# Performance work log

Hardware: AMD Instinct MI355X
Metric: run time of the kernel (lower is better)

## Reference

```python
import jax, jax.numpy as jnp
import numpy as np

N = 50000
E = 800000
D = 128
L = 2


def setup_inputs() -> dict:
    key = jax.random.key(0)
    ks = jax.random.split(key, 8)
    x = jax.random.normal(ks[0], (N, D), dtype=jnp.float32)
    edge_index = jax.random.randint(ks[1], (2, E), 0, N, dtype=jnp.int64)
    s = 1.0 / np.sqrt(D)
    Wl = jax.random.uniform(ks[2], (L, D, D), jnp.float32, -s, s)  # neighbor transform (with bias)
    bl = jax.random.uniform(ks[3], (L, D), jnp.float32, -s, s)
    Wr = jax.random.uniform(ks[4], (L, D, D), jnp.float32, -s, s)  # root/self transform (no bias)
    W = jax.random.uniform(ks[5], (D, D), jnp.float32, -s, s)      # final Linear
    b = jax.random.uniform(ks[6], (D,), jnp.float32, -s, s)
    return {"x": x, "edge_index": edge_index, "Wl": Wl, "bl": bl, "Wr": Wr, "W": W, "b": b}


def reference(x, edge_index, Wl, bl, Wr, W, b):
    src, dst = edge_index[0], edge_index[1]
    n = x.shape[0]
    for l in range(Wl.shape[0]):
        # gather neighbor (source) features, scatter-max into destination nodes
        agg = jax.ops.segment_max(x[src], dst, num_segments=n)  # [N, D]
        agg = jnp.where(jnp.isneginf(agg), 0.0, agg)  # PyG: isolated nodes -> 0
        # SAGEConv: lin_l(agg) + lin_r(x)
        x = agg @ Wl[l].T + bl[l] + x @ Wr[l].T
        x = jax.nn.relu(x)
    return x @ W.T + b
```

## Files before the change

kernel.cpp:

```cpp
#include <hip/hip_runtime.h>
#include <math.h>

#define NN 50000
#define NE 800000
#define DD 128
#define NBUCK 196
#define PTILE 4096
#define PBLOCKS 196
#define CONVB 6250

typedef unsigned short u16;
typedef short s8v __attribute__((ext_vector_type(8)));
typedef float f16v __attribute__((ext_vector_type(16)));

__device__ __forceinline__ u16 f2bf(float f) {
    unsigned u = __float_as_uint(f);
    return (u16)((u + 0x7FFFu + ((u >> 16) & 1u)) >> 16);
}
__device__ __forceinline__ float bflo(unsigned u) { return __uint_as_float(u << 16); }
__device__ __forceinline__ float bfhi(unsigned u) { return __uint_as_float(u & 0xFFFF0000u); }

__device__ __forceinline__ void pack_one(const float* __restrict__ Wl,
                                         const float* __restrict__ Wr,
                                         bool two, int o, u16* __restrict__ out) {
    int j = o & 7;
    int l = (o >> 3) & 63;
    int cn = o >> 9;
    int n = cn & 3;
    int c = cn >> 2;
    int colj = n * 32 + (l & 31);
    int k = c * 16 + (l >> 5) * 8 + j;
    float v;
    if (two) v = (k < DD) ? Wl[colj * DD + k] : Wr[colj * DD + (k - DD)];
    else     v = Wl[colj * DD + k];
    out[o] = f2bf(v);
}

__global__ __launch_bounds__(256) void prep_kernel(
        const float4* __restrict__ x4, ushort4* __restrict__ hb0,
        const float* __restrict__ Wl, const float* __restrict__ Wr,
        const float* __restrict__ W,
        u16* __restrict__ Bpk0, u16* __restrict__ Bpk1, u16* __restrict__ Bpkf,
        int* __restrict__ bcnt) {
    int bid = blockIdx.x;
    int tid = threadIdx.x;
    if (bid < CONVB) {
        int i = bid * 256 + tid;
        float4 v = x4[i];
        ushort4 o;
        o.x = f2bf(v.x); o.y = f2bf(v.y); o.z = f2bf(v.z); o.w = f2bf(v.w);
        hb0[i] = o;
    } else if (bid < CONVB + 128) {
        pack_one(Wl, Wr, true, (bid - CONVB) * 256 + tid, Bpk0);
    } else if (bid < CONVB + 256) {
        pack_one(Wl + DD * DD, Wr + DD * DD, true, (bid - CONVB - 128) * 256 + tid, Bpk1);
    } else if (bid < CONVB + 320) {
        pack_one(W, W, false, (bid - CONVB - 256) * 256 + tid, Bpkf);
    } else {
        if (tid < NBUCK) bcnt[tid] = 0;
    }
}

__global__ __launch_bounds__(256) void bucket_hist(const int* __restrict__ ei,
                                                   int* __restrict__ bcnt) {
    __shared__ int h[NBUCK];
    for (int i = threadIdx.x; i < NBUCK; i += 256) h[i] = 0;
    __syncthreads();
    int e0 = blockIdx.x * PTILE;
#pragma unroll
    for (int i = 0; i < 16; i++) {
        int e = e0 + i * 256 + threadIdx.x;
        if (e < NE) atomicAdd(&h[ei[NE + e] >> 8], 1);
    }
    __syncthreads();
    for (int i = threadIdx.x; i < NBUCK; i += 256)
        if (h[i]) atomicAdd(&bcnt[i], h[i]);
}

__global__ __launch_bounds__(256) void bucket_scan(const int* __restrict__ bcnt,
                                                   int* __restrict__ bbase,
                                                   int* __restrict__ bcur,
                                                   int* __restrict__ rowptr) {
    __shared__ int s[256];
    int t = threadIdx.x;
    int v = (t < NBUCK) ? bcnt[t] : 0;
    s[t] = v;
    __syncthreads();
    for (int o = 1; o < 256; o <<= 1) {
        int u = (t >= o) ? s[t - o] : 0;
        __syncthreads();
        s[t] += u;
        __syncthreads();
    }
    int ex = s[t] - v;
    if (t < NBUCK) { bbase[t] = ex; bcur[t] = ex; }
    if (t == 0) rowptr[NN] = NE;
}

__global__ __launch_bounds__(256) void bucket_partition(const int* __restrict__ ei,
                                                        int* __restrict__ bcur,
                                                        unsigned* __restrict__ packed) {
    __shared__ int h[NBUCK];
    __shared__ int base[NBUCK];
    int t = threadIdx.x;
    for (int i = t; i < NBUCK; i += 256) h[i] = 0;
    __syncthreads();
    int e0 = blockIdx.x * PTILE;
    int dsts[16], srcs[16];
#pragma unroll
    for (int i = 0; i < 16; i++) {
        int e = e0 + i * 256 + t;
        if (e < NE) {
            dsts[i] = ei[NE + e];
            srcs[i] = ei[e];
            atomicAdd(&h[dsts[i] >> 8], 1);
        } else dsts[i] = -1;
    }
    __syncthreads();
    for (int i = t; i < NBUCK; i += 256) {
        int c = h[i];
        base[i] = c ? atomicAdd(&bcur[i], c) : 0;
    }
    __syncthreads();
    for (int i = t; i < NBUCK; i += 256) h[i] = 0;
    __syncthreads();
#pragma unroll
    for (int i = 0; i < 16; i++) {
        if (dsts[i] >= 0) {
            int bk = dsts[i] >> 8;
            int r = atomicAdd(&h[bk], 1);
            packed[base[bk] + r] = (unsigned)srcs[i] | ((unsigned)(dsts[i] & 255) << 16);
        }
    }
}

__global__ __launch_bounds__(256) void bucket_csr(const unsigned* __restrict__ packed,
                                                  const int* __restrict__ bcnt,
                                                  const int* __restrict__ bbase,
                                                  int* __restrict__ rowptr,
                                                  int* __restrict__ col) {
    __shared__ int deg[256];
    __shared__ int off[256];
    int bk = blockIdx.x;
    int cnt = bcnt[bk], base = bbase[bk];
    int t = threadIdx.x;
    deg[t] = 0;
    __syncthreads();
    for (int i = t; i < cnt; i += 256) atomicAdd(&deg[packed[base + i] >> 16], 1);
    __syncthreads();
    int v = deg[t];
    off[t] = v;
    __syncthreads();
    for (int o = 1; o < 256; o <<= 1) {
        int u = (t >= o) ? off[t - o] : 0;
        __syncthreads();
        off[t] += u;
        __syncthreads();
    }
    int ex = off[t] - v;
    int node = (bk << 8) + t;
    if (node < NN) rowptr[node] = base + ex;
    deg[t] = ex;
    __syncthreads();
    for (int i = t; i < cnt; i += 256) {
        unsigned p = packed[base + i];
        int dl = p >> 16;
        int r = atomicAdd(&deg[dl], 1);
        col[base + r] = (int)(p & 0xFFFFu);
    }
}

__device__ __forceinline__ void vmax8(float* m, uint4 v) {
    m[0] = fmaxf(m[0], bflo(v.x)); m[1] = fmaxf(m[1], bfhi(v.x));
    m[2] = fmaxf(m[2], bflo(v.y)); m[3] = fmaxf(m[3], bfhi(v.y));
    m[4] = fmaxf(m[4], bflo(v.z)); m[5] = fmaxf(m[5], bfhi(v.z));
    m[6] = fmaxf(m[6], bflo(v.w)); m[7] = fmaxf(m[7], bfhi(v.w));
}

__global__ __launch_bounds__(256) void agg_kernel_bf(const uint4* __restrict__ xb4,
                                                     const int* __restrict__ row_ptr,
                                                     const int* __restrict__ col,
                                                     uint4* __restrict__ aggb4) {
    int node = blockIdx.x * 16 + (threadIdx.x >> 4);
    if (node >= NN) return;
    int j = threadIdx.x & 15;
    int s0 = row_ptr[node], s1 = row_ptr[node + 1];
    if (s0 == s1) {
        aggb4[(size_t)node * 16 + j] = make_uint4(0, 0, 0, 0);
        return;
    }
    float m0[8], m1[8], m2[8], m3[8];
#pragma unroll
    for (int q = 0; q < 8; q++) { m0[q] = m1[q] = m2[q] = m3[q] = -INFINITY; }
    int i = s0;
    for (; i + 8 <= s1; i += 8) {
        int c0 = col[i],     c1 = col[i + 1], c2 = col[i + 2], c3 = col[i + 3];
        int c4 = col[i + 4], c5 = col[i + 5], c6 = col[i + 6], c7 = col[i + 7];
        uint4 v0 = xb4[(size_t)c0 * 16 + j];
        uint4 v1 = xb4[(size_t)c1 * 16 + j];
        uint4 v2 = xb4[(size_t)c2 * 16 + j];
        uint4 v3 = xb4[(size_t)c3 * 16 + j];
        uint4 v4 = xb4[(size_t)c4 * 16 + j];
        uint4 v5 = xb4[(size_t)c5 * 16 + j];
        uint4 v6 = xb4[(size_t)c6 * 16 + j];
        uint4 v7 = xb4[(size_t)c7 * 16 + j];
        vmax8(m0, v0); vmax8(m1, v1); vmax8(m2, v2); vmax8(m3, v3);
        vmax8(m0, v4); vmax8(m1, v5); vmax8(m2, v6); vmax8(m3, v7);
    }
    for (; i + 4 <= s1; i += 4) {
        int c0 = col[i], c1 = col[i + 1], c2 = col[i + 2], c3 = col[i + 3];
        uint4 v0 = xb4[(size_t)c0 * 16 + j];
        uint4 v1 = xb4[(size_t)c1 * 16 + j];
        uint4 v2 = xb4[(size_t)c2 * 16 + j];
        uint4 v3 = xb4[(size_t)c3 * 16 + j];
        vmax8(m0, v0); vmax8(m1, v1); vmax8(m2, v2); vmax8(m3, v3);
    }
    for (; i < s1; i++) {
        uint4 v = xb4[(size_t)col[i] * 16 + j];
        vmax8(m0, v);
    }
#pragma unroll
    for (int q = 0; q < 8; q++) m0[q] = fmaxf(fmaxf(m0[q], m1[q]), fmaxf(m2[q], m3[q]));
    uint4 o;
    o.x = (__float_as_uint(m0[0]) >> 16) | (__float_as_uint(m0[1]) & 0xFFFF0000u);
    o.y = (__float_as_uint(m0[2]) >> 16) | (__float_as_uint(m0[3]) & 0xFFFF0000u);
    o.z = (__float_as_uint(m0[4]) >> 16) | (__float_as_uint(m0[5]) & 0xFFFF0000u);
    o.w = (__float_as_uint(m0[6]) >> 16) | (__float_as_uint(m0[7]) & 0xFFFF0000u);
    aggb4[(size_t)node * 16 + j] = o;
}

template<int NKC16, bool TWO_SRC, bool RELU, bool OUT_BF16>
__global__ __launch_bounds__(256) void mfma_gemm(const u16* __restrict__ srcA,
                                                 const u16* __restrict__ srcB,
                                                 const u16* __restrict__ Bpk,
                                                 const float* __restrict__ bias,
                                                 void* __restrict__ outv) {
    int tid = threadIdx.x;
    int wt = tid >> 6;
    int lane = tid & 63;
    int row0 = blockIdx.x * 128 + wt * 32;
    int rload = row0 + (lane & 31);
    if (rload > NN - 1) rload = NN - 1;
    int koff = (lane >> 5) * 8;
    const s8v* Bv = (const s8v*)Bpk;

    f16v acc[4];
#pragma unroll
    for (int n = 0; n < 4; n++) acc[n] = (f16v)(0.0f);

#pragma unroll
    for (int c = 0; c < NKC16; c++) {
        const u16* s = srcA;
        int kk = c * 16;
        if (TWO_SRC && c >= 8) { s = srcB; kk = (c - 8) * 16; }
        s8v a = *(const s8v*)(s + (size_t)rload * DD + kk + koff);
#pragma unroll
        for (int n = 0; n < 4; n++) {
            s8v b = Bv[(c * 4 + n) * 64 + lane];
            acc[n] = __builtin_amdgcn_mfma_f32_32x32x16_bf16(a, b, acc[n], 0, 0, 0);
        }
    }

    int rowadd = 4 * (lane >> 5);
#pragma unroll
    for (int n = 0; n < 4; n++) {
        int colj = n * 32 + (lane & 31);
        float bj = bias[colj];
#pragma unroll
        for (int r = 0; r < 16; r++) {
            int row = row0 + (r & 3) + 8 * (r >> 2) + rowadd;
            if (row < NN) {
                float v = acc[n][r] + bj;
                if (RELU) v = fmaxf(v, 0.0f);
                if (OUT_BF16) ((u16*)outv)[(size_t)row * DD + colj] = f2bf(v);
                else          ((float*)outv)[(size_t)row * DD + colj] = v;
            }
        }
    }
}

extern "C" void kernel_launch(void* const* d_in, const int* in_sizes, int n_in,
                              void* d_out, int out_size, void* d_ws, size_t ws_size,
                              hipStream_t stream) {
    const float* x  = (const float*)d_in[0];
    const int*   ei = (const int*)d_in[1];
    const float* Wl = (const float*)d_in[2];
    const float* bl = (const float*)d_in[3];
    const float* Wr = (const float*)d_in[4];
    const float* W  = (const float*)d_in[5];
    const float* b  = (const float*)d_in[6];
    float* out = (float*)d_out;

    u16* aggb = (u16*)d_ws;
    u16* hb0  = aggb + (size_t)NN * DD;
    u16* hb1  = hb0 + (size_t)NN * DD;
    u16* Bpk0 = hb1 + (size_t)NN * DD;
    u16* Bpk1 = Bpk0 + 32768;
    u16* Bpkf = Bpk1 + 32768;
    unsigned* packed = (unsigned*)(Bpkf + 16384);
    int* col    = (int*)(packed + NE);
    int* rowptr = col + NE;
    int* bcnt   = rowptr + NN + 1;
    int* bbase  = bcnt + NBUCK;
    int* bcur   = bbase + NBUCK;

    dim3 blk(256);
    int gemmBlocks = (NN + 127) / 128;
    int aggBlocks  = (NN + 15) / 16;
    int prepBlocks = CONVB + 320 + 1;

    prep_kernel<<<prepBlocks, blk, 0, stream>>>(
        (const float4*)x, (ushort4*)hb0, Wl, Wr, W, Bpk0, Bpk1, Bpkf, bcnt);

    bucket_hist<<<PBLOCKS, blk, 0, stream>>>(ei, bcnt);
    bucket_scan<<<1, blk, 0, stream>>>(bcnt, bbase, bcur, rowptr);
    bucket_partition<<<PBLOCKS, blk, 0, stream>>>(ei, bcur, packed);
    bucket_csr<<<NBUCK, blk, 0, stream>>>(packed, bcnt, bbase, rowptr, col);

    agg_kernel_bf<<<aggBlocks, blk, 0, stream>>>((const uint4*)hb0, rowptr, col, (uint4*)aggb);
    mfma_gemm<16, true, true, true><<<gemmBlocks, blk, 0, stream>>>(
        aggb, hb0, Bpk0, bl, hb1);

    agg_kernel_bf<<<aggBlocks, blk, 0, stream>>>((const uint4*)hb1, rowptr, col, (uint4*)aggb);
    mfma_gemm<16, true, true, true><<<gemmBlocks, blk, 0, stream>>>(
        aggb, hb1, Bpk1, bl + DD, hb0);

    mfma_gemm<8, false, false, false><<<gemmBlocks, blk, 0, stream>>>(
        hb0, nullptr, Bpkf, b, out);
}
```

Measured before the change: 240.6 us.

## Fuse neighbor max-aggregation into layer GEMM and final linear via LDS

Replaces the separate aggregation kernel and GEMM launches with one kernel per layer. Each block gathers the max-aggregated features for its 128 rows into swizzled shared memory, then runs the MFMA GEMM reading A from LDS. The last layer also chains the final linear layer through LDS. This removes the global round trip of the aggregate buffer and two launches, but the gather now runs with far fewer blocks (128 rows each), reducing memory-level parallelism for the latency-bound gather.

```diff
diff --git a/kernel.cpp b/kernel.cpp
--- a/kernel.cpp
+++ b/kernel.cpp
@@ -177,71 +177,83 @@
     m[6] = fmaxf(m[6], bflo(v.w)); m[7] = fmaxf(m[7], bfhi(v.w));
 }
 
-__global__ __launch_bounds__(256) void agg_kernel_bf(const uint4* __restrict__ xb4,
-                                                     const int* __restrict__ row_ptr,
-                                                     const int* __restrict__ col,
-                                                     uint4* __restrict__ aggb4) {
-    int node = blockIdx.x * 16 + (threadIdx.x >> 4);
-    if (node >= NN) return;
-    int j = threadIdx.x & 15;
-    int s0 = row_ptr[node], s1 = row_ptr[node + 1];
-    if (s0 == s1) {
-        aggb4[(size_t)node * 16 + j] = make_uint4(0, 0, 0, 0);
-        return;
-    }
-    float m0[8], m1[8], m2[8], m3[8];
-#pragma unroll
-    for (int q = 0; q < 8; q++) { m0[q] = m1[q] = m2[q] = m3[q] = -INFINITY; }
-    int i = s0;
-    for (; i + 8 <= s1; i += 8) {
-        int c0 = col[i],     c1 = col[i + 1], c2 = col[i + 2], c3 = col[i + 3];
-        int c4 = col[i + 4], c5 = col[i + 5], c6 = col[i + 6], c7 = col[i + 7];
-        uint4 v0 = xb4[(size_t)c0 * 16 + j];
-        uint4 v1 = xb4[(size_t)c1 * 16 + j];
-        uint4 v2 = xb4[(size_t)c2 * 16 + j];
-        uint4 v3 = xb4[(size_t)c3 * 16 + j];
-        uint4 v4 = xb4[(size_t)c4 * 16 + j];
-        uint4 v5 = xb4[(size_t)c5 * 16 + j];
-        uint4 v6 = xb4[(size_t)c6 * 16 + j];
-        uint4 v7 = xb4[(size_t)c7 * 16 + j];
-        vmax8(m0, v0); vmax8(m1, v1); vmax8(m2, v2); vmax8(m3, v3);
-        vmax8(m0, v4); vmax8(m1, v5); vmax8(m2, v6); vmax8(m3, v7);
-    }
-    for (; i + 4 <= s1; i += 4) {
-        int c0 = col[i], c1 = col[i + 1], c2 = col[i + 2], c3 = col[i + 3];
-        uint4 v0 = xb4[(size_t)c0 * 16 + j];
-        uint4 v1 = xb4[(size_t)c1 * 16 + j];
-        uint4 v2 = xb4[(size_t)c2 * 16 + j];
-        uint4 v3 = xb4[(size_t)c3 * 16 + j];
-        vmax8(m0, v0); vmax8(m1, v1); vmax8(m2, v2); vmax8(m3, v3);
-    }
-    for (; i < s1; i++) {
-        uint4 v = xb4[(size_t)col[i] * 16 + j];
-        vmax8(m0, v);
-    }
-#pragma unroll
-    for (int q = 0; q < 8; q++) m0[q] = fmaxf(fmaxf(m0[q], m1[q]), fmaxf(m2[q], m3[q]));
-    uint4 o;
-    o.x = (__float_as_uint(m0[0]) >> 16) | (__float_as_uint(m0[1]) & 0xFFFF0000u);
-    o.y = (__float_as_uint(m0[2]) >> 16) | (__float_as_uint(m0[3]) & 0xFFFF0000u);
-    o.z = (__float_as_uint(m0[4]) >> 16) | (__float_as_uint(m0[5]) & 0xFFFF0000u);
-    o.w = (__float_as_uint(m0[6]) >> 16) | (__float_as_uint(m0[7]) & 0xFFFF0000u);
-    aggb4[(size_t)node * 16 + j] = o;
-}
-
-template<int NKC16, bool TWO_SRC, bool RELU, bool OUT_BF16>
-__global__ __launch_bounds__(256) void mfma_gemm(const u16* __restrict__ srcA,
-                                                 const u16* __restrict__ srcB,
-                                                 const u16* __restrict__ Bpk,
-                                                 const float* __restrict__ bias,
-                                                 void* __restrict__ outv) {
+template<bool FINAL>
+__global__ __launch_bounds__(256) void fused_layer(
+        const u16* __restrict__ hsrc,
+        const int* __restrict__ rowptr,
+        const int* __restrict__ col,
+        const u16* __restrict__ Bpk,
+        const float* __restrict__ bias,
+        const u16* __restrict__ Bpkf,
+        const float* __restrict__ bfin,
+        void* __restrict__ outv) {
+    __shared__ u16 As[128 * 128];
+    char* Ab = (char*)As;
     int tid = threadIdx.x;
+    int row0 = blockIdx.x * 128;
+    const uint4* xb4 = (const uint4*)hsrc;
+
+    {
+        int j = tid & 15;
+        int nl0 = tid >> 4;
+        for (int p = 0; p < 8; p++) {
+            int rl = (p << 4) + nl0;
+            int node = row0 + rl;
+            uint4 o = make_uint4(0u, 0u, 0u, 0u);
+            if (node < NN) {
+                int s0 = rowptr[node], s1 = rowptr[node + 1];
+                if (s0 < s1) {
+                    float m0[8], m1[8], m2[8], m3[8];
+#pragma unroll
+                    for (int q = 0; q < 8; q++) { m0[q] = m1[q] = m2[q] = m3[q] = -INFINITY; }
+                    int i = s0;
+                    for (; i + 8 <= s1; i += 8) {
+                        int c0 = col[i],     c1 = col[i + 1], c2 = col[i + 2], c3 = col[i + 3];
+                        int c4 = col[i + 4], c5 = col[i + 5], c6 = col[i + 6], c7 = col[i + 7];
+                        uint4 v0 = xb4[(size_t)c0 * 16 + j];
+                        uint4 v1 = xb4[(size_t)c1 * 16 + j];
+                        uint4 v2 = xb4[(size_t)c2 * 16 + j];
+                        uint4 v3 = xb4[(size_t)c3 * 16 + j];
+                        uint4 v4 = xb4[(size_t)c4 * 16 + j];
+                        uint4 v5 = xb4[(size_t)c5 * 16 + j];
+                        uint4 v6 = xb4[(size_t)c6 * 16 + j];
+                        uint4 v7 = xb4[(size_t)c7 * 16 + j];
+                        vmax8(m0, v0); vmax8(m1, v1); vmax8(m2, v2); vmax8(m3, v3);
+                        vmax8(m0, v4); vmax8(m1, v5); vmax8(m2, v6); vmax8(m3, v7);
+                    }
+                    for (; i + 4 <= s1; i += 4) {
+                        int c0 = col[i], c1 = col[i + 1], c2 = col[i + 2], c3 = col[i + 3];
+                        uint4 v0 = xb4[(size_t)c0 * 16 + j];
+                        uint4 v1 = xb4[(size_t)c1 * 16 + j];
+                        uint4 v2 = xb4[(size_t)c2 * 16 + j];
+                        uint4 v3 = xb4[(size_t)c3 * 16 + j];
+                        vmax8(m0, v0); vmax8(m1, v1); vmax8(m2, v2); vmax8(m3, v3);
+                    }
+                    for (; i < s1; i++) {
+                        uint4 v = xb4[(size_t)col[i] * 16 + j];
+                        vmax8(m0, v);
+                    }
+#pragma unroll
+                    for (int q = 0; q < 8; q++)
+                        m0[q] = fmaxf(fmaxf(m0[q], m1[q]), fmaxf(m2[q], m3[q]));
+                    o.x = (__float_as_uint(m0[0]) >> 16) | (__float_as_uint(m0[1]) & 0xFFFF0000u);
+                    o.y = (__float_as_uint(m0[2]) >> 16) | (__float_as_uint(m0[3]) & 0xFFFF0000u);
+                    o.z = (__float_as_uint(m0[4]) >> 16) | (__float_as_uint(m0[5]) & 0xFFFF0000u);
+                    o.w = (__float_as_uint(m0[6]) >> 16) | (__float_as_uint(m0[7]) & 0xFFFF0000u);
+                }
+            }
+            *(uint4*)(Ab + rl * 256 + ((j << 4) ^ ((rl & 7) << 4))) = o;
+        }
+    }
+    __syncthreads();
+
     int wt = tid >> 6;
     int lane = tid & 63;
-    int row0 = blockIdx.x * 128 + wt * 32;
-    int rload = row0 + (lane & 31);
-    if (rload > NN - 1) rload = NN - 1;
+    int arl = wt * 32 + (lane & 31);
+    int rg = row0 + arl;
+    if (rg > NN - 1) rg = NN - 1;
     int koff = (lane >> 5) * 8;
+    int swz = (arl & 7) << 4;
     const s8v* Bv = (const s8v*)Bpk;
 
     f16v acc[4];
@@ -249,11 +261,12 @@
     for (int n = 0; n < 4; n++) acc[n] = (f16v)(0.0f);
 
 #pragma unroll
-    for (int c = 0; c < NKC16; c++) {
-        const u16* s = srcA;
-        int kk = c * 16;
-        if (TWO_SRC && c >= 8) { s = srcB; kk = (c - 8) * 16; }
-        s8v a = *(const s8v*)(s + (size_t)rload * DD + kk + koff);
+    for (int c = 0; c < 16; c++) {
+        s8v a;
+        if (c < 8)
+            a = *(const s8v*)(Ab + arl * 256 + (((c * 16 + koff) * 2) ^ swz));
+        else
+            a = *(const s8v*)(hsrc + (size_t)rg * DD + (c - 8) * 16 + koff);
 #pragma unroll
         for (int n = 0; n < 4; n++) {
             s8v b = Bv[(c * 4 + n) * 64 + lane];
@@ -262,18 +275,56 @@
     }
 
     int rowadd = 4 * (lane >> 5);
-#pragma unroll
-    for (int n = 0; n < 4; n++) {
-        int colj = n * 32 + (lane & 31);
-        float bj = bias[colj];
-#pragma unroll
-        for (int r = 0; r < 16; r++) {
-            int row = row0 + (r & 3) + 8 * (r >> 2) + rowadd;
-            if (row < NN) {
-                float v = acc[n][r] + bj;
-                if (RELU) v = fmaxf(v, 0.0f);
-                if (OUT_BF16) ((u16*)outv)[(size_t)row * DD + colj] = f2bf(v);
-                else          ((float*)outv)[(size_t)row * DD + colj] = v;
+    if constexpr (!FINAL) {
+        u16* hdst = (u16*)outv;
+#pragma unroll
+        for (int n = 0; n < 4; n++) {
+            int colj = n * 32 + (lane & 31);
+            float bj = bias[colj];
+#pragma unroll
+            for (int r = 0; r < 16; r++) {
+                int row = row0 + wt * 32 + (r & 3) + 8 * (r >> 2) + rowadd;
+                if (row < NN)
+                    hdst[(size_t)row * DD + colj] = f2bf(fmaxf(acc[n][r] + bj, 0.0f));
+            }
+        }
+    } else {
+        __syncthreads();
+#pragma unroll
+        for (int n = 0; n < 4; n++) {
+            int colj = n * 32 + (lane & 31);
+            float bj = bias[colj];
+#pragma unroll
+            for (int r = 0; r < 16; r++) {
+                int rloc = wt * 32 + (r & 3) + 8 * (r >> 2) + rowadd;
+                float v = fmaxf(acc[n][r] + bj, 0.0f);
+                *(u16*)(Ab + rloc * 256 + ((colj * 2) ^ ((rloc & 7) << 4))) = f2bf(v);
+            }
+        }
+        __syncthreads();
+        const s8v* Bvf = (const s8v*)Bpkf;
+        f16v acc2[4];
+#pragma unroll
+        for (int n = 0; n < 4; n++) acc2[n] = (f16v)(0.0f);
+#pragma unroll
+        for (int c = 0; c < 8; c++) {
+            s8v a = *(const s8v*)(Ab + arl * 256 + (((c * 16 + koff) * 2) ^ swz));
+#pragma unroll
+            for (int n = 0; n < 4; n++) {
+                s8v b = Bvf[(c * 4 + n) * 64 + lane];
+                acc2[n] = __builtin_amdgcn_mfma_f32_32x32x16_bf16(a, b, acc2[n], 0, 0, 0);
+            }
+        }
+        float* fout = (float*)outv;
+#pragma unroll
+        for (int n = 0; n < 4; n++) {
+            int colj = n * 32 + (lane & 31);
+            float bj = bfin[colj];
+#pragma unroll
+            for (int r = 0; r < 16; r++) {
+                int row = row0 + wt * 32 + (r & 3) + 8 * (r >> 2) + rowadd;
+                if (row < NN)
+                    fout[(size_t)row * DD + colj] = acc2[n][r] + bj;
             }
         }
     }
@@ -306,7 +357,6 @@
 
     dim3 blk(256);
     int gemmBlocks = (NN + 127) / 128;
-    int aggBlocks  = (NN + 15) / 16;
     int prepBlocks = CONVB + 320 + 1;
 
     prep_kernel<<<prepBlocks, blk, 0, stream>>>(
@@ -317,14 +367,9 @@
     bucket_partition<<<PBLOCKS, blk, 0, stream>>>(ei, bcur, packed);
     bucket_csr<<<NBUCK, blk, 0, stream>>>(packed, bcnt, bbase, rowptr, col);
 
-    agg_kernel_bf<<<aggBlocks, blk, 0, stream>>>((const uint4*)hb0, rowptr, col, (uint4*)aggb);
-    mfma_gemm<16, true, true, true><<<gemmBlocks, blk, 0, stream>>>(
-        aggb, hb0, Bpk0, bl, hb1);
-
-    agg_kernel_bf<<<aggBlocks, blk, 0, stream>>>((const uint4*)hb1, rowptr, col, (uint4*)aggb);
-    mfma_gemm<16, true, true, true><<<gemmBlocks, blk, 0, stream>>>(
-        aggb, hb1, Bpk1, bl + DD, hb0);
-
-    mfma_gemm<8, false, false, false><<<gemmBlocks, blk, 0, stream>>>(
-        hb0, nullptr, Bpkf, b, out);
-}
+    fused_layer<false><<<gemmBlocks, blk, 0, stream>>>(
+        hb0, rowptr, col, Bpk0, bl, nullptr, nullptr, hb1);
+
+    fused_layer<true><<<gemmBlocks, blk, 0, stream>>>(
+        hb1, rowptr, col, Bpk1, bl + DD, Bpkf, b, out);
+}
```

After: 247.8 us. 3.0% more time.
